# Kernel optimization log

Measured on AMD Instinct MI355X. Metric: run time of the kernel, lower is better.

The kernel has to match this reference:

```python
import jax, jax.numpy as jnp
import numpy as np

B, T, D, H = 128, 512, 256, 512


def setup_inputs() -> dict:
    key = jax.random.key(0)
    ks = jax.random.split(key, 16)
    s = 0.02
    return {
        "x": jax.random.normal(ks[0], (B, T, D), dtype=jnp.float32),
        "proj_w": jax.random.normal(ks[1], (D, D), dtype=jnp.float32) * s,
        "proj_b": jnp.zeros((D,), dtype=jnp.float32),
        "wx0": jax.random.normal(ks[2], (4 * H, D), dtype=jnp.float32) * s,
        "bx0": jnp.zeros((4 * H,), dtype=jnp.float32),
        "wh0": jax.random.normal(ks[3], (4 * H, H), dtype=jnp.float32) * s,
        "bh0": jnp.zeros((4 * H,), dtype=jnp.float32),
        "wx1": jax.random.normal(ks[4], (4 * H, H), dtype=jnp.float32) * s,
        "bx1": jnp.zeros((4 * H,), dtype=jnp.float32),
        "wh1": jax.random.normal(ks[5], (4 * H, H), dtype=jnp.float32) * s,
        "bh1": jnp.zeros((4 * H,), dtype=jnp.float32),
        "fc1_w": jax.random.normal(ks[6], (32, H), dtype=jnp.float32) * s,
        "fc1_b": jnp.zeros((32,), dtype=jnp.float32),
        "fc2_w": jax.random.normal(ks[7], (1, 32), dtype=jnp.float32) * s,
        "fc2_b": jnp.zeros((1,), dtype=jnp.float32),
    }


def _cell(x_t, h, c, wx, bx, wh, bh):
    gates = x_t @ wx.T + bx + h @ wh.T + bh  # [B, 4H]
    i, f, g, o = jnp.split(gates, 4, axis=1)
    c_new = jax.nn.sigmoid(f) * c + jax.nn.sigmoid(i) * jnp.tanh(g)
    h_new = jax.nn.sigmoid(o) * jnp.tanh(c_new)
    return h_new, c_new


def reference(x, proj_w, proj_b, wx0, bx0, wh0, bh0, wx1, bx1, wh1, bh1,
              fc1_w, fc1_b, fc2_w, fc2_b):
    b = x.shape[0]
    h = wh0.shape[1]
    xp = x @ proj_w.T + proj_b  # input_projection, [B,T,D]
    xs = jnp.swapaxes(xp, 0, 1)  # [T,B,D] for scan over time

    def step(carry, x_t):
        h0, c0, h1, c1 = carry
        h0, c0 = _cell(x_t, h0, c0, wx0, bx0, wh0, bh0)
        h1, c1 = _cell(h0, h1, c1, wx1, bx1, wh1, bh1)
        return (h0, c0, h1, c1), None

    z = jnp.zeros((b, h), dtype=x.dtype)
    (h0, c0, h1, c1), _ = jax.lax.scan(step, (z, z, z, z), xs)
    hid = jax.nn.relu(h1 @ fc1_w.T + fc1_b)
    return hid @ fc2_w.T + fc2_b  # [B,1]
```

## Files before the change

### kernel.cpp

```cpp
#include <hip/hip_runtime.h>

#define BB 128
#define TT 512
#define DD 256
#define HH 512

__device__ __forceinline__ float sig_(float x) { return 1.0f / (1.0f + __expf(-x)); }

#define FMA4(ACC, AV, WV)                     \
  do {                                        \
    ACC[0] = fmaf((AV), (WV).x, ACC[0]);      \
    ACC[1] = fmaf((AV), (WV).y, ACC[1]);      \
    ACC[2] = fmaf((AV), (WV).z, ACC[2]);      \
    ACC[3] = fmaf((AV), (WV).w, ACC[3]);      \
  } while (0)

__device__ float g_c[2 * BB * HH];

__global__ __launch_bounds__(256) void proj_kernel(const float* __restrict__ x,
                                                   const float* __restrict__ pw,
                                                   const float* __restrict__ pb,
                                                   float* __restrict__ xp) {
  __shared__ float At[64 * 68];
  __shared__ float Bt[64 * 68];
  const int bm = blockIdx.x >> 2;
  const int bn = blockIdx.x & 3;
  const int tid = threadIdx.x;
  const int rg = tid >> 4;
  const int cgi = tid & 15;
  const int m0 = bm * 64, n0 = bn * 64;
  float acc[4][4] = {};
  for (int kt = 0; kt < 4; ++kt) {
    const int k0 = kt * 64;
    {
      const int r = tid >> 2, q = tid & 3;
      const float4* src = (const float4*)(x + (size_t)(m0 + r) * DD + k0 + q * 16);
      float4* dst = (float4*)&At[r * 68 + q * 16];
#pragma unroll
      for (int j = 0; j < 4; ++j) dst[j] = src[j];
    }
    {
      const int n = tid & 63, kg = tid >> 6;
      const float4* src = (const float4*)(pw + (size_t)(n0 + n) * DD + k0 + kg * 16);
#pragma unroll
      for (int j = 0; j < 4; ++j) {
        float4 v = src[j];
        const int kk = kg * 16 + j * 4;
        Bt[(kk + 0) * 68 + n] = v.x;
        Bt[(kk + 1) * 68 + n] = v.y;
        Bt[(kk + 2) * 68 + n] = v.z;
        Bt[(kk + 3) * 68 + n] = v.w;
      }
    }
    __syncthreads();
#pragma unroll
    for (int k4 = 0; k4 < 64; k4 += 4) {
      float4 a[4], b[4];
#pragma unroll
      for (int j = 0; j < 4; ++j) a[j] = *(const float4*)&At[(rg * 4 + j) * 68 + k4];
#pragma unroll
      for (int j = 0; j < 4; ++j) b[j] = *(const float4*)&Bt[(k4 + j) * 68 + cgi * 4];
#pragma unroll
      for (int jr = 0; jr < 4; ++jr) {
        FMA4(acc[jr], a[jr].x, b[0]);
        FMA4(acc[jr], a[jr].y, b[1]);
        FMA4(acc[jr], a[jr].z, b[2]);
        FMA4(acc[jr], a[jr].w, b[3]);
      }
    }
    __syncthreads();
  }
  const float4 bias = *(const float4*)&pb[n0 + cgi * 4];
#pragma unroll
  for (int jr = 0; jr < 4; ++jr) {
    float4 o;
    o.x = acc[jr][0] + bias.x;
    o.y = acc[jr][1] + bias.y;
    o.z = acc[jr][2] + bias.z;
    o.w = acc[jr][3] + bias.w;
    *(float4*)&xp[(size_t)(m0 + rg * 4 + jr) * DD + n0 + cgi * 4] = o;
  }
}


__device__ __forceinline__ void load_plain(float4 (&R)[8], const float* base,
                                           size_t rs, int trb, int gq) {
#pragma unroll
  for (int j = 0; j < 8; ++j)
    R[j] = *(const float4*)(base + (size_t)(j * 16 + trb) * rs + (gq << 2));
}

__device__ __forceinline__ void write_tile(float* Abuf, const float4 (&R)[8],
                                           int trb, int wp_) {
#pragma unroll
  for (int j = 0; j < 8; ++j)
    *(float4*)&Abuf[(j * 16 + trb) * 64 + (wp_ << 2)] = R[j];
}

__device__ __forceinline__ void compute_tile(float acc0[4], float acc1[4],
                                             const float* Abuf, const float* Wl,
                                             int kt, int rowg, int cell) {
  const float* Wt = Wl + (kt << 10) + (cell << 2);
  const float* Ar = Abuf + rowg * 128;
  const int rsw = rowg & 7;
#pragma unroll
  for (int k4 = 0; k4 < 64; k4 += 4) {
    const int off = (((k4 >> 2) ^ rsw) << 2);
    const float4 a0 = *(const float4*)(Ar + off);
    const float4 a1 = *(const float4*)(Ar + 64 + off);
    const float* wp = Wt + (k4 << 4);
    const float4 w0 = *(const float4*)(wp + 0);
    const float4 w1 = *(const float4*)(wp + 16);
    const float4 w2 = *(const float4*)(wp + 32);
    const float4 w3 = *(const float4*)(wp + 48);
    FMA4(acc0, a0.x, w0);
    FMA4(acc0, a0.y, w1);
    FMA4(acc0, a0.z, w2);
    FMA4(acc0, a0.w, w3);
    FMA4(acc1, a1.x, w0);
    FMA4(acc1, a1.y, w1);
    FMA4(acc1, a1.z, w2);
    FMA4(acc1, a1.w, w3);
  }
}

__global__ __launch_bounds__(256, 1) void lstm_phase(
    const float* __restrict__ xp,
    const float* __restrict__ wx0, const float* __restrict__ bx0,
    const float* __restrict__ wh0, const float* __restrict__ bh0,
    const float* __restrict__ wx1, const float* __restrict__ bx1,
    const float* __restrict__ wh1, const float* __restrict__ bh1,
    float* __restrict__ h0buf, float* __restrict__ h1buf, int p) {
  __shared__ float Wl[16384];
  __shared__ float Ab[2][8192];

  const int bidx = blockIdx.x;
  const int role = bidx >> 7;
  const bool active = role ? (p >= 1) : (p < TT);
  if (!active) return;

  const int bj = bidx & 127;
  const int tid = threadIdx.x;
  const int cell = tid & 3;
  const int rowg = tid >> 2;
  const int trb = tid >> 4;
  const int gq = tid & 15;
  const int wp_ = gq ^ ((trb >> 1) & 7);
  const int cell_g = bj * 4 + cell;

  const float* __restrict__ wx = role ? wx1 : wx0;
  const float* __restrict__ wh = role ? wh1 : wh0;
  const float* __restrict__ bxv = role ? bx1 : bx0;
  const float* __restrict__ bhv = role ? bh1 : bh0;
  const int KX = role ? HH : DD;
  const int nt = (KX + HH) >> 6;

  {
    const int col = tid & 15, part = tid >> 4;
    const int lc = col >> 2, g = col & 3;
    const int grow = g * HH + bj * 4 + lc;
    const int span = (KX + HH) >> 4;
    const int k0 = part * span;
    for (int k = k0; k < k0 + span; k += 4) {
      float4 v;
      if (k < KX) v = *(const float4*)(wx + (size_t)grow * KX + k);
      else        v = *(const float4*)(wh + (size_t)grow * HH + (k - KX));
      Wl[(k + 0) * 16 + col] = v.x;
      Wl[(k + 1) * 16 + col] = v.y;
      Wl[(k + 2) * 16 + col] = v.z;
      Wl[(k + 3) * 16 + col] = v.w;
    }
  }

  float bg[4];
#pragma unroll
  for (int g = 0; g < 4; ++g)
    bg[g] = bxv[(size_t)g * HH + cell_g] + bhv[(size_t)g * HH + cell_g];

  const int t = role ? (p - 1) : p;
  const int rd = (p + 1) & 1;
  const int wr = p & 1;
  const float* __restrict__ h0rd = h0buf + (size_t)rd * BB * HH;
  const float* __restrict__ h1rd = h1buf + (size_t)rd * BB * HH;
  float* __restrict__ hout = (role ? h1buf : h0buf) + (size_t)wr * BB * HH;

  const bool first = role ? (p == 1) : (p == 0);
  float* __restrict__ cslot0 = &g_c[((size_t)role * BB + rowg * 2 + 0) * HH + cell_g];
  float* __restrict__ cslot1 = &g_c[((size_t)role * BB + rowg * 2 + 1) * HH + cell_g];
  const float cst0 = first ? 0.0f : *cslot0;
  const float cst1 = first ? 0.0f : *cslot1;

  float acc0[4] = {0.f, 0.f, 0.f, 0.f};
  float acc1[4] = {0.f, 0.f, 0.f, 0.f};

  auto srcload = [&](float4(&R)[8], int kt) {
    if (role == 0) {
      if (kt < 4)
        load_plain(R, xp + (size_t)t * DD + kt * 64, (size_t)TT * DD, trb, gq);
      else
        load_plain(R, h0rd + (kt - 4) * 64, (size_t)HH, trb, gq);
    } else {
      if (kt < 8) load_plain(R, h0rd + kt * 64, (size_t)HH, trb, gq);
      else        load_plain(R, h1rd + (kt - 8) * 64, (size_t)HH, trb, gq);
    }
  };

  float4 ra[8], rb4[8];
  srcload(ra, 0);
  __syncthreads();
#pragma unroll 1
  for (int kt = 0; kt < nt; kt += 2) {
    srcload(rb4, kt + 1);
    write_tile(Ab[0], ra, trb, wp_);
    __syncthreads();
    compute_tile(acc0, acc1, Ab[0], Wl, kt, rowg, cell);
    if (kt + 2 < nt) srcload(ra, kt + 2);
    __syncthreads();
    write_tile(Ab[1], rb4, trb, wp_);
    __syncthreads();
    compute_tile(acc0, acc1, Ab[1], Wl, kt + 1, rowg, cell);
    __syncthreads();
  }

  {
    float iv = acc0[0] + bg[0], fv = acc0[1] + bg[1];
    float gv = acc0[2] + bg[2], ov = acc0[3] + bg[3];
    float cn = sig_(fv) * cst0 + sig_(iv) * tanhf(gv);
    *cslot0 = cn;
    hout[(size_t)(rowg * 2 + 0) * HH + cell_g] = sig_(ov) * tanhf(cn);
    iv = acc1[0] + bg[0]; fv = acc1[1] + bg[1];
    gv = acc1[2] + bg[2]; ov = acc1[3] + bg[3];
    cn = sig_(fv) * cst1 + sig_(iv) * tanhf(gv);
    *cslot1 = cn;
    hout[(size_t)(rowg * 2 + 1) * HH + cell_g] = sig_(ov) * tanhf(cn);
  }
}

__global__ __launch_bounds__(256) void head_kernel(const float* __restrict__ h1,
                                                   const float* __restrict__ fc1w,
                                                   const float* __restrict__ fc1b,
                                                   const float* __restrict__ fc2w,
                                                   const float* __restrict__ fc2b,
                                                   float* __restrict__ out) {
  __shared__ float part[256];
  __shared__ float hid[32];
  const int r = blockIdx.x;
  const int tid = threadIdx.x;
  const int c = tid & 31, pt = tid >> 5;
  const float4* ha = (const float4*)(h1 + (size_t)r * HH + pt * 64);
  const float4* wa = (const float4*)(fc1w + (size_t)c * HH + pt * 64);
  float s = 0.f;
#pragma unroll
  for (int j = 0; j < 16; ++j) {
    float4 av = ha[j], wv = wa[j];
    s = fmaf(av.x, wv.x, s);
    s = fmaf(av.y, wv.y, s);
    s = fmaf(av.z, wv.z, s);
    s = fmaf(av.w, wv.w, s);
  }
  part[tid] = s;
  __syncthreads();
  if (tid < 32) {
    float v = fc1b[tid];
#pragma unroll
    for (int q = 0; q < 8; ++q) v += part[q * 32 + tid];
    hid[tid] = fmaxf(v, 0.f);
  }
  __syncthreads();
  if (tid == 0) {
    float v = fc2b[0];
    for (int cc = 0; cc < 32; ++cc) v = fmaf(hid[cc], fc2w[cc], v);
    out[r] = v;
  }
}

extern "C" void kernel_launch(void* const* d_in, const int* in_sizes, int n_in,
                              void* d_out, int out_size, void* d_ws, size_t ws_size,
                              hipStream_t stream) {
  const float* x    = (const float*)d_in[0];
  const float* pw   = (const float*)d_in[1];
  const float* pb   = (const float*)d_in[2];
  const float* wx0  = (const float*)d_in[3];
  const float* bx0  = (const float*)d_in[4];
  const float* wh0  = (const float*)d_in[5];
  const float* bh0  = (const float*)d_in[6];
  const float* wx1  = (const float*)d_in[7];
  const float* bx1  = (const float*)d_in[8];
  const float* wh1  = (const float*)d_in[9];
  const float* bh1  = (const float*)d_in[10];
  const float* fc1w = (const float*)d_in[11];
  const float* fc1b = (const float*)d_in[12];
  const float* fc2w = (const float*)d_in[13];
  const float* fc2b = (const float*)d_in[14];
  float* out = (float*)d_out;

  float* xp = (float*)d_ws;
  float* h0buf = xp + (size_t)BB * TT * DD;
  float* h1buf = h0buf + 2 * BB * HH;

  hipMemsetAsync(h0buf, 0, (size_t)4 * BB * HH * sizeof(float), stream);

  proj_kernel<<<dim3(4096), dim3(256), 0, stream>>>(x, pw, pb, xp);

  for (int p = 0; p <= TT; ++p) {
    lstm_phase<<<dim3(256), dim3(256), 0, stream>>>(
        xp, wx0, bx0, wh0, bh0, wx1, bx1, wh1, bh1, h0buf, h1buf, p);
  }

  head_kernel<<<dim3(BB), dim3(256), 0, stream>>>(h1buf, fc1w, fc1b, fc2w, fc2b, out);
}
```

Baseline: 36.44 ms.

## Pre-pack LSTM weights per cell and read them from global instead of LDS

A new pack_w kernel runs once per call and reorders wx/wh for both layers into a per-cell contiguous, gate-interleaved layout in a global buffer. Each of the 513 per-timestep lstm_phase launches then reads weights straight from that buffer (through the caches) instead of gathering and transposing them into shared memory at the start of every launch. This removes the per-launch strided weight gather and the 64KB of LDS per block. The cost is that the inner loop now issues global/L2 weight loads in place of LDS reads, and the barrier placement in the double-buffered loop is reworked.

Result: slower. 86.50 ms (+137.4%).

```diff
diff --git a/kernel.cpp b/kernel.cpp
--- a/kernel.cpp
+++ b/kernel.cpp
@@ -16,6 +16,11 @@
   } while (0)
 
 __device__ float g_c[2 * BB * HH];
+
+#define W0_CELL 3072
+#define W1_CELL 4096
+#define W1_BASE (512 * W0_CELL)
+__device__ float g_w[512 * W0_CELL + 512 * W1_CELL];
 
 __global__ __launch_bounds__(256) void proj_kernel(const float* __restrict__ x,
                                                    const float* __restrict__ pw,
@@ -82,6 +87,33 @@
   }
 }
 
+__global__ __launch_bounds__(256) void pack_w(
+    const float* __restrict__ wx0, const float* __restrict__ wh0,
+    const float* __restrict__ wx1, const float* __restrict__ wh1) {
+  const int role = blockIdx.x >> 9;
+  const int c = blockIdx.x & 511;
+  const int KX = role ? HH : DD;
+  const int nk4 = (KX + HH) >> 2;
+  const float* __restrict__ wx = role ? wx1 : wx0;
+  const float* __restrict__ wh = role ? wh1 : wh0;
+  float* __restrict__ dst =
+      g_w + (role ? (W1_BASE + (size_t)c * W1_CELL) : ((size_t)c * W0_CELL));
+  for (int k4 = threadIdx.x; k4 < nk4; k4 += 256) {
+    const int k = k4 << 2;
+#pragma unroll
+    for (int g = 0; g < 4; ++g) {
+      const int row = g * HH + c;
+      float4 v;
+      if (k < KX) v = *(const float4*)(wx + (size_t)row * KX + k);
+      else        v = *(const float4*)(wh + (size_t)row * HH + (k - KX));
+      dst[k4 * 16 + 0 * 4 + g] = v.x;
+      dst[k4 * 16 + 1 * 4 + g] = v.y;
+      dst[k4 * 16 + 2 * 4 + g] = v.z;
+      dst[k4 * 16 + 3 * 4 + g] = v.w;
+    }
+  }
+}
+
 
 __device__ __forceinline__ void load_plain(float4 (&R)[8], const float* base,
                                            size_t rs, int trb, int gq) {
@@ -98,9 +130,9 @@
 }
 
 __device__ __forceinline__ void compute_tile(float acc0[4], float acc1[4],
-                                             const float* Abuf, const float* Wl,
-                                             int kt, int rowg, int cell) {
-  const float* Wt = Wl + (kt << 10) + (cell << 2);
+                                             const float* Abuf,
+                                             const float* __restrict__ wt,
+                                             int rowg) {
   const float* Ar = Abuf + rowg * 128;
   const int rsw = rowg & 7;
 #pragma unroll
@@ -108,11 +140,11 @@
     const int off = (((k4 >> 2) ^ rsw) << 2);
     const float4 a0 = *(const float4*)(Ar + off);
     const float4 a1 = *(const float4*)(Ar + 64 + off);
-    const float* wp = Wt + (k4 << 4);
+    const float* wp = wt + (k4 << 2);
     const float4 w0 = *(const float4*)(wp + 0);
-    const float4 w1 = *(const float4*)(wp + 16);
-    const float4 w2 = *(const float4*)(wp + 32);
-    const float4 w3 = *(const float4*)(wp + 48);
+    const float4 w1 = *(const float4*)(wp + 4);
+    const float4 w2 = *(const float4*)(wp + 8);
+    const float4 w3 = *(const float4*)(wp + 12);
     FMA4(acc0, a0.x, w0);
     FMA4(acc0, a0.y, w1);
     FMA4(acc0, a0.z, w2);
@@ -126,12 +158,9 @@
 
 __global__ __launch_bounds__(256, 1) void lstm_phase(
     const float* __restrict__ xp,
-    const float* __restrict__ wx0, const float* __restrict__ bx0,
-    const float* __restrict__ wh0, const float* __restrict__ bh0,
-    const float* __restrict__ wx1, const float* __restrict__ bx1,
-    const float* __restrict__ wh1, const float* __restrict__ bh1,
+    const float* __restrict__ bx0, const float* __restrict__ bh0,
+    const float* __restrict__ bx1, const float* __restrict__ bh1,
     float* __restrict__ h0buf, float* __restrict__ h1buf, int p) {
-  __shared__ float Wl[16384];
   __shared__ float Ab[2][8192];
 
   const int bidx = blockIdx.x;
@@ -148,29 +177,14 @@
   const int wp_ = gq ^ ((trb >> 1) & 7);
   const int cell_g = bj * 4 + cell;
 
-  const float* __restrict__ wx = role ? wx1 : wx0;
-  const float* __restrict__ wh = role ? wh1 : wh0;
   const float* __restrict__ bxv = role ? bx1 : bx0;
   const float* __restrict__ bhv = role ? bh1 : bh0;
   const int KX = role ? HH : DD;
   const int nt = (KX + HH) >> 6;
 
-  {
-    const int col = tid & 15, part = tid >> 4;
-    const int lc = col >> 2, g = col & 3;
-    const int grow = g * HH + bj * 4 + lc;
-    const int span = (KX + HH) >> 4;
-    const int k0 = part * span;
-    for (int k = k0; k < k0 + span; k += 4) {
-      float4 v;
-      if (k < KX) v = *(const float4*)(wx + (size_t)grow * KX + k);
-      else        v = *(const float4*)(wh + (size_t)grow * HH + (k - KX));
-      Wl[(k + 0) * 16 + col] = v.x;
-      Wl[(k + 1) * 16 + col] = v.y;
-      Wl[(k + 2) * 16 + col] = v.z;
-      Wl[(k + 3) * 16 + col] = v.w;
-    }
-  }
+  const float* __restrict__ wbase =
+      g_w + (role ? (W1_BASE + (size_t)cell_g * W1_CELL)
+                  : ((size_t)cell_g * W0_CELL));
 
   float bg[4];
 #pragma unroll
@@ -185,10 +199,13 @@
   float* __restrict__ hout = (role ? h1buf : h0buf) + (size_t)wr * BB * HH;
 
   const bool first = role ? (p == 1) : (p == 0);
-  float* __restrict__ cslot0 = &g_c[((size_t)role * BB + rowg * 2 + 0) * HH + cell_g];
-  float* __restrict__ cslot1 = &g_c[((size_t)role * BB + rowg * 2 + 1) * HH + cell_g];
-  const float cst0 = first ? 0.0f : *cslot0;
-  const float cst1 = first ? 0.0f : *cslot1;
+  float cst0, cst1;
+  {
+    float* c0 = &g_c[((size_t)role * BB + rowg * 2 + 0) * HH + cell_g];
+    float* c1 = &g_c[((size_t)role * BB + rowg * 2 + 1) * HH + cell_g];
+    cst0 = first ? 0.0f : *c0;
+    cst1 = first ? 0.0f : *c1;
+  }
 
   float acc0[4] = {0.f, 0.f, 0.f, 0.f};
   float acc1[4] = {0.f, 0.f, 0.f, 0.f};
@@ -207,31 +224,30 @@
 
   float4 ra[8], rb4[8];
   srcload(ra, 0);
-  __syncthreads();
 #pragma unroll 1
   for (int kt = 0; kt < nt; kt += 2) {
     srcload(rb4, kt + 1);
+    __syncthreads();
     write_tile(Ab[0], ra, trb, wp_);
     __syncthreads();
-    compute_tile(acc0, acc1, Ab[0], Wl, kt, rowg, cell);
+    compute_tile(acc0, acc1, Ab[0], wbase + (size_t)kt * 256, rowg);
     if (kt + 2 < nt) srcload(ra, kt + 2);
     __syncthreads();
     write_tile(Ab[1], rb4, trb, wp_);
     __syncthreads();
-    compute_tile(acc0, acc1, Ab[1], Wl, kt + 1, rowg, cell);
-    __syncthreads();
+    compute_tile(acc0, acc1, Ab[1], wbase + (size_t)(kt + 1) * 256, rowg);
   }
 
   {
     float iv = acc0[0] + bg[0], fv = acc0[1] + bg[1];
     float gv = acc0[2] + bg[2], ov = acc0[3] + bg[3];
     float cn = sig_(fv) * cst0 + sig_(iv) * tanhf(gv);
-    *cslot0 = cn;
+    g_c[((size_t)role * BB + rowg * 2 + 0) * HH + cell_g] = cn;
     hout[(size_t)(rowg * 2 + 0) * HH + cell_g] = sig_(ov) * tanhf(cn);
     iv = acc1[0] + bg[0]; fv = acc1[1] + bg[1];
     gv = acc1[2] + bg[2]; ov = acc1[3] + bg[3];
     cn = sig_(fv) * cst1 + sig_(iv) * tanhf(gv);
-    *cslot1 = cn;
+    g_c[((size_t)role * BB + rowg * 2 + 1) * HH + cell_g] = cn;
     hout[(size_t)(rowg * 2 + 1) * HH + cell_g] = sig_(ov) * tanhf(cn);
   }
 }
@@ -300,11 +316,12 @@
 
   hipMemsetAsync(h0buf, 0, (size_t)4 * BB * HH * sizeof(float), stream);
 
+  pack_w<<<dim3(1024), dim3(256), 0, stream>>>(wx0, wh0, wx1, wh1);
   proj_kernel<<<dim3(4096), dim3(256), 0, stream>>>(x, pw, pb, xp);
 
   for (int p = 0; p <= TT; ++p) {
     lstm_phase<<<dim3(256), dim3(256), 0, stream>>>(
-        xp, wx0, bx0, wh0, bh0, wx1, bx1, wh1, bh1, h0buf, h1buf, p);
+        xp, bx0, bh0, bx1, bh1, h0buf, h1buf, p);
   }
 
   head_kernel<<<dim3(BB), dim3(256), 0, stream>>>(h1buf, fc1w, fc1b, fc2w, fc2b, out);
```

## Prepack LSTM weights into per-block contiguous layout and cut barriers in K loop

Applied to the files above, without the earlier changes.

A new pack_w kernel transposes and gathers each block's gate weight slice once per forward call into a contiguous global buffer. Each of the 513 per-timestep launches then copies that slice into shared memory with coalesced float4 loads, replacing the strided gather and scalar scattered LDS writes. The first activation tile load is issued before the weight copy so the two overlap. The double-buffered K loop is reordered to use two barriers per pair of tiles instead of four, writing the next tile while computing the current one. The cost is an extra global buffer of about 3.5M floats and one more kernel launch.

Measured after the change: 37.12 ms. No clear change (+1.9%).

```diff
diff --git a/kernel.cpp b/kernel.cpp
--- a/kernel.cpp
+++ b/kernel.cpp
@@ -16,6 +16,11 @@
   } while (0)
 
 __device__ float g_c[2 * BB * HH];
+
+#define W0_BLK 12288
+#define W1_BLK 16384
+#define W1_BASE (128 * W0_BLK)
+__device__ float g_w[128 * W0_BLK + 128 * W1_BLK];
 
 __global__ __launch_bounds__(256) void proj_kernel(const float* __restrict__ x,
                                                    const float* __restrict__ pw,
@@ -82,6 +87,33 @@
   }
 }
 
+__global__ __launch_bounds__(256) void pack_w(
+    const float* __restrict__ wx0, const float* __restrict__ wh0,
+    const float* __restrict__ wx1, const float* __restrict__ wh1) {
+  const int role = blockIdx.x >> 7;
+  const int bj = blockIdx.x & 127;
+  const int tid = threadIdx.x;
+  const int KX = role ? HH : DD;
+  const float* __restrict__ wx = role ? wx1 : wx0;
+  const float* __restrict__ wh = role ? wh1 : wh0;
+  float* __restrict__ dst =
+      g_w + (role ? (W1_BASE + (size_t)bj * W1_BLK) : ((size_t)bj * W0_BLK));
+  const int col = tid & 15, part = tid >> 4;
+  const int lc = col >> 2, g = col & 3;
+  const int grow = g * HH + bj * 4 + lc;
+  const int span = (KX + HH) >> 4;
+  const int k0 = part * span;
+  for (int k = k0; k < k0 + span; k += 4) {
+    float4 v;
+    if (k < KX) v = *(const float4*)(wx + (size_t)grow * KX + k);
+    else        v = *(const float4*)(wh + (size_t)grow * HH + (k - KX));
+    dst[(k + 0) * 16 + col] = v.x;
+    dst[(k + 1) * 16 + col] = v.y;
+    dst[(k + 2) * 16 + col] = v.z;
+    dst[(k + 3) * 16 + col] = v.w;
+  }
+}
+
 
 __device__ __forceinline__ void load_plain(float4 (&R)[8], const float* base,
                                            size_t rs, int trb, int gq) {
@@ -126,10 +158,8 @@
 
 __global__ __launch_bounds__(256, 1) void lstm_phase(
     const float* __restrict__ xp,
-    const float* __restrict__ wx0, const float* __restrict__ bx0,
-    const float* __restrict__ wh0, const float* __restrict__ bh0,
-    const float* __restrict__ wx1, const float* __restrict__ bx1,
-    const float* __restrict__ wh1, const float* __restrict__ bh1,
+    const float* __restrict__ bx0, const float* __restrict__ bh0,
+    const float* __restrict__ bx1, const float* __restrict__ bh1,
     float* __restrict__ h0buf, float* __restrict__ h1buf, int p) {
   __shared__ float Wl[16384];
   __shared__ float Ab[2][8192];
@@ -148,34 +178,10 @@
   const int wp_ = gq ^ ((trb >> 1) & 7);
   const int cell_g = bj * 4 + cell;
 
-  const float* __restrict__ wx = role ? wx1 : wx0;
-  const float* __restrict__ wh = role ? wh1 : wh0;
   const float* __restrict__ bxv = role ? bx1 : bx0;
   const float* __restrict__ bhv = role ? bh1 : bh0;
   const int KX = role ? HH : DD;
   const int nt = (KX + HH) >> 6;
-
-  {
-    const int col = tid & 15, part = tid >> 4;
-    const int lc = col >> 2, g = col & 3;
-    const int grow = g * HH + bj * 4 + lc;
-    const int span = (KX + HH) >> 4;
-    const int k0 = part * span;
-    for (int k = k0; k < k0 + span; k += 4) {
-      float4 v;
-      if (k < KX) v = *(const float4*)(wx + (size_t)grow * KX + k);
-      else        v = *(const float4*)(wh + (size_t)grow * HH + (k - KX));
-      Wl[(k + 0) * 16 + col] = v.x;
-      Wl[(k + 1) * 16 + col] = v.y;
-      Wl[(k + 2) * 16 + col] = v.z;
-      Wl[(k + 3) * 16 + col] = v.w;
-    }
-  }
-
-  float bg[4];
-#pragma unroll
-  for (int g = 0; g < 4; ++g)
-    bg[g] = bxv[(size_t)g * HH + cell_g] + bhv[(size_t)g * HH + cell_g];
 
   const int t = role ? (p - 1) : p;
   const int rd = (p + 1) & 1;
@@ -183,15 +189,6 @@
   const float* __restrict__ h0rd = h0buf + (size_t)rd * BB * HH;
   const float* __restrict__ h1rd = h1buf + (size_t)rd * BB * HH;
   float* __restrict__ hout = (role ? h1buf : h0buf) + (size_t)wr * BB * HH;
-
-  const bool first = role ? (p == 1) : (p == 0);
-  float* __restrict__ cslot0 = &g_c[((size_t)role * BB + rowg * 2 + 0) * HH + cell_g];
-  float* __restrict__ cslot1 = &g_c[((size_t)role * BB + rowg * 2 + 1) * HH + cell_g];
-  const float cst0 = first ? 0.0f : *cslot0;
-  const float cst1 = first ? 0.0f : *cslot1;
-
-  float acc0[4] = {0.f, 0.f, 0.f, 0.f};
-  float acc1[4] = {0.f, 0.f, 0.f, 0.f};
 
   auto srcload = [&](float4(&R)[8], int kt) {
     if (role == 0) {
@@ -207,17 +204,44 @@
 
   float4 ra[8], rb4[8];
   srcload(ra, 0);
+
+  {
+    const float4* __restrict__ wsrc = (const float4*)(
+        g_w + (role ? (W1_BASE + (size_t)bj * W1_BLK) : ((size_t)bj * W0_BLK)));
+    float4* __restrict__ wdst = (float4*)Wl;
+    const int n4 = (KX + HH) << 2;
+    for (int i = tid; i < n4; i += 256) wdst[i] = wsrc[i];
+  }
+
+  float bg[4];
+#pragma unroll
+  for (int g = 0; g < 4; ++g)
+    bg[g] = bxv[(size_t)g * HH + cell_g] + bhv[(size_t)g * HH + cell_g];
+
+  const bool first = role ? (p == 1) : (p == 0);
+  float cst0, cst1;
+  {
+    float* c0 = &g_c[((size_t)role * BB + rowg * 2 + 0) * HH + cell_g];
+    float* c1 = &g_c[((size_t)role * BB + rowg * 2 + 1) * HH + cell_g];
+    cst0 = first ? 0.0f : *c0;
+    cst1 = first ? 0.0f : *c1;
+  }
+
+  float acc0[4] = {0.f, 0.f, 0.f, 0.f};
+  float acc1[4] = {0.f, 0.f, 0.f, 0.f};
+
+  srcload(rb4, 1);
+  write_tile(Ab[0], ra, trb, wp_);
   __syncthreads();
+
 #pragma unroll 1
   for (int kt = 0; kt < nt; kt += 2) {
-    srcload(rb4, kt + 1);
-    write_tile(Ab[0], ra, trb, wp_);
+    if (kt + 2 < nt) srcload(ra, kt + 2);
+    write_tile(Ab[1], rb4, trb, wp_);
+    compute_tile(acc0, acc1, Ab[0], Wl, kt, rowg, cell);
     __syncthreads();
-    compute_tile(acc0, acc1, Ab[0], Wl, kt, rowg, cell);
-    if (kt + 2 < nt) srcload(ra, kt + 2);
-    __syncthreads();
-    write_tile(Ab[1], rb4, trb, wp_);
-    __syncthreads();
+    if (kt + 3 < nt) srcload(rb4, kt + 3);
+    if (kt + 2 < nt) write_tile(Ab[0], ra, trb, wp_);
     compute_tile(acc0, acc1, Ab[1], Wl, kt + 1, rowg, cell);
     __syncthreads();
   }
@@ -226,12 +250,12 @@
     float iv = acc0[0] + bg[0], fv = acc0[1] + bg[1];
     float gv = acc0[2] + bg[2], ov = acc0[3] + bg[3];
     float cn = sig_(fv) * cst0 + sig_(iv) * tanhf(gv);
-    *cslot0 = cn;
+    g_c[((size_t)role * BB + rowg * 2 + 0) * HH + cell_g] = cn;
     hout[(size_t)(rowg * 2 + 0) * HH + cell_g] = sig_(ov) * tanhf(cn);
     iv = acc1[0] + bg[0]; fv = acc1[1] + bg[1];
     gv = acc1[2] + bg[2]; ov = acc1[3] + bg[3];
     cn = sig_(fv) * cst1 + sig_(iv) * tanhf(gv);
-    *cslot1 = cn;
+    g_c[((size_t)role * BB + rowg * 2 + 1) * HH + cell_g] = cn;
     hout[(size_t)(rowg * 2 + 1) * HH + cell_g] = sig_(ov) * tanhf(cn);
   }
 }
@@ -300,11 +324,12 @@
 
   hipMemsetAsync(h0buf, 0, (size_t)4 * BB * HH * sizeof(float), stream);
 
+  pack_w<<<dim3(256), dim3(256), 0, stream>>>(wx0, wh0, wx1, wh1);
   proj_kernel<<<dim3(4096), dim3(256), 0, stream>>>(x, pw, pb, xp);
 
   for (int p = 0; p <= TT; ++p) {
     lstm_phase<<<dim3(256), dim3(256), 0, stream>>>(
-        xp, wx0, bx0, wh0, bh0, wx1, bx1, wh1, bh1, h0buf, h1buf, p);
+        xp, bx0, bh0, bx1, bh1, h0buf, h1buf, p);
   }
 
   head_kernel<<<dim3(BB), dim3(256), 0, stream>>>(h1buf, fc1w, fc1b, fc2w, fc2b, out);
```
